# Performance work log

Measured on AMD Instinct MI355X. Metric: run time of the kernel, lower is better.

Reference implementation:

```python
import jax, jax.numpy as jnp
import numpy as np

B, N, D, H, O, K, N_USER, C = 1, 4096, 64, 4, 64, 2, 4000, 2


def setup_inputs() -> dict:
    key = jax.random.key(0)
    ks = jax.random.split(key, 7)
    h = jax.random.normal(ks[0], (B, N, D), jnp.float32)
    # dense 0/1 adjacency per heterogeneous kind, with self-loops so no row is empty
    adj = jax.random.randint(ks[1], (K, B, N, N), 0, 2).astype(jnp.float32)
    hadj = jnp.maximum(adj, jnp.eye(N, dtype=jnp.float32))
    s = 1.0 / np.sqrt(D).astype(np.float32)
    w = jax.random.normal(ks[2], (K, H, D, O), jnp.float32) * s
    a_src = jax.random.normal(ks[3], (K, H, O, 1), jnp.float32) * (1.0 / np.sqrt(O).astype(np.float32))
    a_dst = jax.random.normal(ks[4], (K, H, O, 1), jnp.float32) * (1.0 / np.sqrt(O).astype(np.float32))
    fc_w = jax.random.normal(ks[5], (C, O * K), jnp.float32) * (1.0 / np.sqrt(O * K).astype(np.float32))
    fc_b = jnp.zeros((C,), jnp.float32)
    return {"h": h, "hadj": hadj, "w": w, "a_src": a_src, "a_dst": a_dst, "fc_w": fc_w, "fc_b": fc_b}


def _gat(h, adj, w_k, a_src_k, a_dst_k):
    # h: (B,N,D); adj: (B,N,N); w_k: (H,D,O); a_*: (H,O,1)
    h_prime = jnp.einsum('bnf,hfo->bhno', h, w_k)          # (B,H,N,O)
    t = jnp.tanh(h_prime)
    attn_src = jnp.einsum('bhno,hoi->bhni', t, a_src_k)    # (B,H,N,1)
    attn_dst = jnp.einsum('bhno,hoi->bhni', t, a_dst_k)    # (B,H,N,1)
    attn = attn_src + jnp.swapaxes(attn_dst, -1, -2)       # (B,H,N,N) broadcast add
    attn = jnp.where(attn >= 0, attn, 0.2 * attn)          # LeakyReLU(0.2)
    attn = jnp.where(adj[:, None] > 0, attn, -jnp.inf)     # dense mask
    attn = jax.nn.softmax(attn, axis=-1)                   # dropout is a no-op in eval
    out = jnp.einsum('bhnm,bhmo->bhno', attn, h_prime)     # (B,H,N,O)
    return out.mean(axis=1)                                # mean over heads -> (B,N,O)


def reference(h, hadj, w, a_src, a_dst, fc_w, fc_b):
    embs = []
    for k in range(K):  # small fixed loop over heterogeneous node kinds
        x = _gat(h, hadj[k], w[k], a_src[k], a_dst[k])
        embs.append(x[:, :N_USER])
    type_aware = jnp.concatenate(embs, axis=-1)            # (B, N_USER, K*O)
    logits = type_aware @ fc_w.T + fc_b                    # (B, N_USER, C)
    return jax.nn.log_softmax(logits, axis=-1)
```

## Files before the change

### kernel.cpp

```cpp
#include <hip/hip_runtime.h>
#include <math.h>

constexpr int KK = 2;
constexpr int HH = 4;
constexpr int NN = 4096;
constexpr int DD = 64;
constexpr int OO = 64;
constexpr int NU = 4000;
constexpr int CC = 2;
constexpr float LOG2E = 1.44269504088896340736f;

typedef float vf4 __attribute__((ext_vector_type(4)));
typedef float vf2 __attribute__((ext_vector_type(2)));

__device__ __forceinline__ float fexp2(float x) {
#if __has_builtin(__builtin_amdgcn_exp2f)
  return __builtin_amdgcn_exp2f(x);
#else
  return exp2f(x);
#endif
}
__device__ __forceinline__ float frcp(float x) {
#if __has_builtin(__builtin_amdgcn_rcpf)
  return __builtin_amdgcn_rcpf(x);
#else
  return 1.0f / x;
#endif
}
__device__ __forceinline__ float ftanh(float x) {
  float e = fexp2(x * (2.0f * LOG2E));
  return 1.0f - 2.0f * frcp(e + 1.0f);
}

__global__ __launch_bounds__(256) void gat_phase1(
    const float* __restrict__ hsrc, const float* __restrict__ w,
    const float* __restrict__ a_src, const float* __restrict__ a_dst,
    const float* __restrict__ fc_w,
    float* __restrict__ srcAA, float* __restrict__ Bp,
    float* __restrict__ B5p, float* __restrict__ g0p,
    float* __restrict__ g1p) {
  const int kh = blockIdx.y;
  const int k = kh >> 2;
  const int i0 = blockIdx.x * 32;
  const int tid = threadIdx.x;

  __shared__ float w_s[DD][OO];
  __shared__ float hs_un[DD * 36];

  {
    const vf4* wp = (const vf4*)(w + (size_t)kh * DD * OO);
    vf4* ws4 = (vf4*)w_s;
    for (int t = tid; t < DD * OO / 4; t += 256) ws4[t] = wp[t];
  }
  for (int t = tid; t < 512; t += 256) {
    const int row = t >> 4;
    const int f4 = (t & 15) * 4;
    vf4 v = *(const vf4*)(hsrc + (size_t)(i0 + row) * DD + f4);
    hs_un[(f4 + 0) * 36 + row] = v.x;
    hs_un[(f4 + 1) * 36 + row] = v.y;
    hs_un[(f4 + 2) * 36 + row] = v.z;
    hs_un[(f4 + 3) * 36 + row] = v.w;
  }
  __syncthreads();

  const int og = tid & 15;
  const int rg = tid >> 4;
  const int o0 = og * 4;
  const int r0 = rg * 2;

  float hp[2][4];
#pragma unroll
  for (int j = 0; j < 2; ++j)
#pragma unroll
    for (int u = 0; u < 4; ++u) hp[j][u] = 0.0f;

#pragma unroll 8
  for (int f = 0; f < DD; ++f) {
    vf2 hv = *(const vf2*)&hs_un[f * 36 + r0];
    vf4 wv = *(const vf4*)&w_s[f][o0];
    hp[0][0] = fmaf(hv.x, wv.x, hp[0][0]);
    hp[0][1] = fmaf(hv.x, wv.y, hp[0][1]);
    hp[0][2] = fmaf(hv.x, wv.z, hp[0][2]);
    hp[0][3] = fmaf(hv.x, wv.w, hp[0][3]);
    hp[1][0] = fmaf(hv.y, wv.x, hp[1][0]);
    hp[1][1] = fmaf(hv.y, wv.y, hp[1][1]);
    hp[1][2] = fmaf(hv.y, wv.z, hp[1][2]);
    hp[1][3] = fmaf(hv.y, wv.w, hp[1][3]);
  }

  float as[4], ad[4], f0[4], f1[4];
#pragma unroll
  for (int u = 0; u < 4; ++u) {
    as[u] = a_src[kh * OO + o0 + u];
    ad[u] = a_dst[kh * OO + o0 + u];
    f0[u] = fc_w[0 * (KK * OO) + k * OO + o0 + u];
    f1[u] = fc_w[1 * (KK * OO) + k * OO + o0 + u];
  }

  float vals[2][4];
#pragma unroll
  for (int j = 0; j < 2; ++j) {
    float sp = 0.0f, dp = 0.0f, g0 = 0.0f, g1 = 0.0f;
#pragma unroll
    for (int u = 0; u < 4; ++u) {
      float v = hp[j][u];
      float t = ftanh(v);
      sp = fmaf(t, as[u], sp);
      dp = fmaf(t, ad[u], dp);
      g0 = fmaf(v, f0[u], g0);
      g1 = fmaf(v, f1[u], g1);
    }
    vals[j][0] = sp;
    vals[j][1] = dp;
    vals[j][2] = g0;
    vals[j][3] = g1;
  }
  __syncthreads();

#pragma unroll
  for (int j = 0; j < 2; ++j) {
#pragma unroll
    for (int v = 0; v < 4; ++v)
      hs_un[(v * 32 + r0 + j) * 17 + og] = vals[j][v];
  }
  __syncthreads();

  if (tid < 128) {
    const int val = tid & 3;
    const int j2 = tid >> 2;
    const float* pr = &hs_un[(val * 32 + j2) * 17];
    vf4 s0 = *(const vf4*)(pr + 0);
    vf4 s1 = *(const vf4*)(pr + 4);
    vf4 s2 = *(const vf4*)(pr + 8);
    vf4 s3 = *(const vf4*)(pr + 12);
    vf4 t4 = s0 + s1 + s2 + s3;
    float sum = t4.x + t4.y + t4.z + t4.w;
    const size_t idx = (size_t)kh * NN + i0 + j2;
    if (val == 0) {
      float sp = sum * LOG2E;
      vf2 v = {fexp2(sp), fexp2(0.2f * sp)};
      *(vf2*)(srcAA + idx * 2) = v;
    } else if (val == 1) {
      float dp = sum * LOG2E;
      Bp[idx] = fexp2(dp);
      B5p[idx] = fexp2(0.2f * dp);
    } else if (val == 2) {
      g0p[idx] = sum;
    } else {
      g1p[idx] = sum;
    }
  }
}

__global__ __launch_bounds__(256) void gat_phase2(
    const float* __restrict__ adj, const float* __restrict__ srcAA,
    const float* __restrict__ Bp, const float* __restrict__ B5p,
    const float* __restrict__ g0p, const float* __restrict__ g1p,
    float* __restrict__ S) {
  const int k = blockIdx.y;
  const int r0 = blockIdx.x * 4;
  const int tid = threadIdx.x;
  const int wave = tid >> 6;
  const int lane = tid & 63;

  float A[4][4], A5[4][4];
#pragma unroll
  for (int h = 0; h < 4; ++h) {
    const float* base = srcAA + ((size_t)(k * HH + h) * NN + r0) * 2;
#pragma unroll
    for (int r = 0; r < 4; ++r) {
      A[r][h] = base[r * 2 + 0];
      A5[r][h] = base[r * 2 + 1];
    }
  }

  float l[4][4], a0[4][4], a1[4][4];
#pragma unroll
  for (int r = 0; r < 4; ++r)
#pragma unroll
    for (int h = 0; h < 4; ++h) {
      l[r][h] = 0.0f;
      a0[r][h] = 0.0f;
      a1[r][h] = 0.0f;
    }

  const float* adjk = adj + (size_t)k * NN * NN;
  const int jw = wave * 1024 + lane * 4;

  vf4 avc[4], avn[4];
#pragma unroll
  for (int r = 0; r < 4; ++r)
    avc[r] = *(const vf4*)(adjk + (size_t)(r0 + r) * NN + jw);

#pragma unroll 1
  for (int t = 0; t < 4; ++t) {
    const int j = jw + t * 256;
    if (t < 3) {
#pragma unroll
      for (int r = 0; r < 4; ++r)
        avn[r] = *(const vf4*)(adjk + (size_t)(r0 + r) * NN + j + 256);
    }
    size_t pb = (size_t)(k * HH + 0) * NN + j;
    vf4 bC = *(const vf4*)(Bp + pb);
    vf4 b5C = *(const vf4*)(B5p + pb);
    vf4 g0C = *(const vf4*)(g0p + pb);
    vf4 g1C = *(const vf4*)(g1p + pb);
#pragma unroll
    for (int h = 0; h < 4; ++h) {
      vf4 b = bC, b5 = b5C, g0 = g0C, g1 = g1C;
      if (h < 3) {
        size_t pn = (size_t)(k * HH + h + 1) * NN + j;
        bC = *(const vf4*)(Bp + pn);
        b5C = *(const vf4*)(B5p + pn);
        g0C = *(const vf4*)(g0p + pn);
        g1C = *(const vf4*)(g1p + pn);
      }
      vf2 blo = {b.x, b.y}, bhi = {b.z, b.w};
      vf2 b5lo = {b5.x, b5.y}, b5hi = {b5.z, b5.w};
#pragma unroll
      for (int r = 0; r < 4; ++r) {
        vf2 elo = __builtin_elementwise_max(blo * A[r][h], b5lo * A5[r][h]);
        vf2 ehi = __builtin_elementwise_max(bhi * A[r][h], b5hi * A5[r][h]);
        float p0 = elo.x * avc[r].x;
        float p1 = elo.y * avc[r].y;
        float p2 = ehi.x * avc[r].z;
        float p3 = ehi.y * avc[r].w;
        l[r][h] += (p0 + p1) + (p2 + p3);
        a0[r][h] = fmaf(p0, g0.x, fmaf(p1, g0.y, fmaf(p2, g0.z, fmaf(p3, g0.w, a0[r][h]))));
        a1[r][h] = fmaf(p0, g1.x, fmaf(p1, g1.y, fmaf(p2, g1.z, fmaf(p3, g1.w, a1[r][h]))));
      }
    }
#pragma unroll
    for (int r = 0; r < 4; ++r) avc[r] = avn[r];
  }

  float red[4][4][3];
#pragma unroll
  for (int r = 0; r < 4; ++r)
#pragma unroll
    for (int h = 0; h < 4; ++h) {
      float x0 = l[r][h], x1 = a0[r][h], x2 = a1[r][h];
#pragma unroll
      for (int off = 32; off > 0; off >>= 1) {
        x0 += __shfl_xor(x0, off, 64);
        x1 += __shfl_xor(x1, off, 64);
        x2 += __shfl_xor(x2, off, 64);
      }
      red[r][h][0] = x0;
      red[r][h][1] = x1;
      red[r][h][2] = x2;
    }

  __shared__ float sred[4][48];
  if (lane == 0) {
#pragma unroll
    for (int r = 0; r < 4; ++r)
#pragma unroll
      for (int h = 0; h < 4; ++h) {
#pragma unroll
        for (int c = 0; c < 3; ++c)
          sred[wave][(r * 4 + h) * 3 + c] = red[r][h][c];
      }
  }
  __syncthreads();
  if (tid < 8) {
    const int r = tid >> 1, c = tid & 1;
    float acc = 0.0f;
#pragma unroll
    for (int h = 0; h < 4; ++h) {
      const int vb = (r * 4 + h) * 3;
      float ls = sred[0][vb] + sred[1][vb] + sred[2][vb] + sred[3][vb];
      float ac = sred[0][vb + 1 + c] + sred[1][vb + 1 + c] +
                 sred[2][vb + 1 + c] + sred[3][vb + 1 + c];
      acc += ac / ls;
    }
    S[((size_t)k * NU + r0 + r) * CC + c] = 0.25f * acc;
  }
}

__global__ __launch_bounds__(256) void gat_phase3(
    const float* __restrict__ S, const float* __restrict__ fc_b,
    float* __restrict__ out) {
  const int i = blockIdx.x * 256 + threadIdx.x;
  if (i >= NU) return;
  float l0 = S[(size_t)i * CC + 0] + S[((size_t)NU + i) * CC + 0] + fc_b[0];
  float l1 = S[(size_t)i * CC + 1] + S[((size_t)NU + i) * CC + 1] + fc_b[1];
  float m = fmaxf(l0, l1);
  float lse = m + logf(expf(l0 - m) + expf(l1 - m));
  out[i * CC + 0] = l0 - lse;
  out[i * CC + 1] = l1 - lse;
}

extern "C" void kernel_launch(void* const* d_in, const int* in_sizes, int n_in,
                              void* d_out, int out_size, void* d_ws, size_t ws_size,
                              hipStream_t stream) {
  const float* hsrc  = (const float*)d_in[0];
  const float* hadj  = (const float*)d_in[1];
  const float* w     = (const float*)d_in[2];
  const float* a_src = (const float*)d_in[3];
  const float* a_dst = (const float*)d_in[4];
  const float* fc_w  = (const float*)d_in[5];
  const float* fc_b  = (const float*)d_in[6];
  float* out = (float*)d_out;

  char* ws = (char*)d_ws;
  float* srcAA = (float*)(ws + 0);
  float* Bp    = (float*)(ws + 262144);
  float* B5p   = (float*)(ws + 393216);
  float* g0p   = (float*)(ws + 524288);
  float* g1p   = (float*)(ws + 655360);
  float* S     = (float*)(ws + 786432);

  dim3 g1(NN / 32, KK * HH);
  gat_phase1<<<g1, 256, 0, stream>>>(hsrc, w, a_src, a_dst, fc_w,
                                     srcAA, Bp, B5p, g0p, g1p);
  dim3 g2(NU / 4, KK);
  gat_phase2<<<g2, 256, 0, stream>>>(hadj, srcAA, Bp, B5p, g0p, g1p, S);
  gat_phase3<<<(NU + 255) / 256, 256, 0, stream>>>(S, fc_b, out);
}
```

Measured before the change: 235.6 us.

## Split phase2 into single-wave blocks per column chunk, reduce partials in phase3

Result: no change. 235.7 us (+0.1%).

```diff
diff --git a/kernel.cpp b/kernel.cpp
--- a/kernel.cpp
+++ b/kernel.cpp
@@ -8,6 +8,7 @@
 constexpr int OO = 64;
 constexpr int NU = 4000;
 constexpr int CC = 2;
+constexpr int JSPLIT = 4;
 constexpr float LOG2E = 1.44269504088896340736f;
 
 typedef float vf4 __attribute__((ext_vector_type(4)));
@@ -41,42 +42,43 @@
     float* __restrict__ g1p) {
   const int kh = blockIdx.y;
   const int k = kh >> 2;
-  const int i0 = blockIdx.x * 32;
+  const int i0 = blockIdx.x * 64;
   const int tid = threadIdx.x;
 
+  __shared__ float h_s[DD][68];
   __shared__ float w_s[DD][OO];
-  __shared__ float hs_un[DD * 36];
+  __shared__ float part[4][64][17];
 
   {
     const vf4* wp = (const vf4*)(w + (size_t)kh * DD * OO);
     vf4* ws4 = (vf4*)w_s;
     for (int t = tid; t < DD * OO / 4; t += 256) ws4[t] = wp[t];
   }
-  for (int t = tid; t < 512; t += 256) {
+  for (int t = tid; t < 1024; t += 256) {
     const int row = t >> 4;
     const int f4 = (t & 15) * 4;
     vf4 v = *(const vf4*)(hsrc + (size_t)(i0 + row) * DD + f4);
-    hs_un[(f4 + 0) * 36 + row] = v.x;
-    hs_un[(f4 + 1) * 36 + row] = v.y;
-    hs_un[(f4 + 2) * 36 + row] = v.z;
-    hs_un[(f4 + 3) * 36 + row] = v.w;
+    h_s[f4 + 0][row] = v.x;
+    h_s[f4 + 1][row] = v.y;
+    h_s[f4 + 2][row] = v.z;
+    h_s[f4 + 3][row] = v.w;
   }
   __syncthreads();
 
   const int og = tid & 15;
   const int rg = tid >> 4;
   const int o0 = og * 4;
-  const int r0 = rg * 2;
-
-  float hp[2][4];
-#pragma unroll
-  for (int j = 0; j < 2; ++j)
+  const int r0 = rg * 4;
+
+  float hp[4][4];
+#pragma unroll
+  for (int j = 0; j < 4; ++j)
 #pragma unroll
     for (int u = 0; u < 4; ++u) hp[j][u] = 0.0f;
 
 #pragma unroll 8
   for (int f = 0; f < DD; ++f) {
-    vf2 hv = *(const vf2*)&hs_un[f * 36 + r0];
+    vf4 hv = *(const vf4*)&h_s[f][r0];
     vf4 wv = *(const vf4*)&w_s[f][o0];
     hp[0][0] = fmaf(hv.x, wv.x, hp[0][0]);
     hp[0][1] = fmaf(hv.x, wv.y, hp[0][1]);
@@ -86,6 +88,14 @@
     hp[1][1] = fmaf(hv.y, wv.y, hp[1][1]);
     hp[1][2] = fmaf(hv.y, wv.z, hp[1][2]);
     hp[1][3] = fmaf(hv.y, wv.w, hp[1][3]);
+    hp[2][0] = fmaf(hv.z, wv.x, hp[2][0]);
+    hp[2][1] = fmaf(hv.z, wv.y, hp[2][1]);
+    hp[2][2] = fmaf(hv.z, wv.z, hp[2][2]);
+    hp[2][3] = fmaf(hv.z, wv.w, hp[2][3]);
+    hp[3][0] = fmaf(hv.w, wv.x, hp[3][0]);
+    hp[3][1] = fmaf(hv.w, wv.y, hp[3][1]);
+    hp[3][2] = fmaf(hv.w, wv.z, hp[3][2]);
+    hp[3][3] = fmaf(hv.w, wv.w, hp[3][3]);
   }
 
   float as[4], ad[4], f0[4], f1[4];
@@ -97,9 +107,8 @@
     f1[u] = fc_w[1 * (KK * OO) + k * OO + o0 + u];
   }
 
-  float vals[2][4];
-#pragma unroll
-  for (int j = 0; j < 2; ++j) {
+#pragma unroll
+  for (int j = 0; j < 4; ++j) {
     float sp = 0.0f, dp = 0.0f, g0 = 0.0f, g1 = 0.0f;
 #pragma unroll
     for (int u = 0; u < 4; ++u) {
@@ -110,25 +119,17 @@
       g0 = fmaf(v, f0[u], g0);
       g1 = fmaf(v, f1[u], g1);
     }
-    vals[j][0] = sp;
-    vals[j][1] = dp;
-    vals[j][2] = g0;
-    vals[j][3] = g1;
+    part[0][r0 + j][og] = sp;
+    part[1][r0 + j][og] = dp;
+    part[2][r0 + j][og] = g0;
+    part[3][r0 + j][og] = g1;
   }
   __syncthreads();
 
-#pragma unroll
-  for (int j = 0; j < 2; ++j) {
-#pragma unroll
-    for (int v = 0; v < 4; ++v)
-      hs_un[(v * 32 + r0 + j) * 17 + og] = vals[j][v];
-  }
-  __syncthreads();
-
-  if (tid < 128) {
+  {
     const int val = tid & 3;
     const int j2 = tid >> 2;
-    const float* pr = &hs_un[(val * 32 + j2) * 17];
+    const float* pr = &part[val][j2][0];
     vf4 s0 = *(const vf4*)(pr + 0);
     vf4 s1 = *(const vf4*)(pr + 4);
     vf4 s2 = *(const vf4*)(pr + 8);
@@ -152,16 +153,15 @@
   }
 }
 
-__global__ __launch_bounds__(256) void gat_phase2(
+__global__ __launch_bounds__(64) void gat_phase2(
     const float* __restrict__ adj, const float* __restrict__ srcAA,
     const float* __restrict__ Bp, const float* __restrict__ B5p,
     const float* __restrict__ g0p, const float* __restrict__ g1p,
-    float* __restrict__ S) {
-  const int k = blockIdx.y;
+    float* __restrict__ P) {
+  const int k = blockIdx.y >> 2;
+  const int chunk = blockIdx.y & 3;
   const int r0 = blockIdx.x * 4;
-  const int tid = threadIdx.x;
-  const int wave = tid >> 6;
-  const int lane = tid & 63;
+  const int lane = threadIdx.x;
 
   float A[4][4], A5[4][4];
 #pragma unroll
@@ -185,7 +185,7 @@
     }
 
   const float* adjk = adj + (size_t)k * NN * NN;
-  const int jw = wave * 1024 + lane * 4;
+  const int jw = chunk * 1024 + lane * 4;
 
   vf4 avc[4], avn[4];
 #pragma unroll
@@ -234,7 +234,6 @@
     for (int r = 0; r < 4; ++r) avc[r] = avn[r];
   }
 
-  float red[4][4][3];
 #pragma unroll
   for (int r = 0; r < 4; ++r)
 #pragma unroll
@@ -246,45 +245,48 @@
         x1 += __shfl_xor(x1, off, 64);
         x2 += __shfl_xor(x2, off, 64);
       }
-      red[r][h][0] = x0;
-      red[r][h][1] = x1;
-      red[r][h][2] = x2;
-    }
-
-  __shared__ float sred[4][48];
+      l[r][h] = x0;
+      a0[r][h] = x1;
+      a1[r][h] = x2;
+    }
+
   if (lane == 0) {
 #pragma unroll
     for (int r = 0; r < 4; ++r)
 #pragma unroll
       for (int h = 0; h < 4; ++h) {
-#pragma unroll
-        for (int c = 0; c < 3; ++c)
-          sred[wave][(r * 4 + h) * 3 + c] = red[r][h][c];
-      }
-  }
-  __syncthreads();
-  if (tid < 8) {
-    const int r = tid >> 1, c = tid & 1;
-    float acc = 0.0f;
-#pragma unroll
-    for (int h = 0; h < 4; ++h) {
-      const int vb = (r * 4 + h) * 3;
-      float ls = sred[0][vb] + sred[1][vb] + sred[2][vb] + sred[3][vb];
-      float ac = sred[0][vb + 1 + c] + sred[1][vb + 1 + c] +
-                 sred[2][vb + 1 + c] + sred[3][vb + 1 + c];
-      acc += ac / ls;
-    }
-    S[((size_t)k * NU + r0 + r) * CC + c] = 0.25f * acc;
+        size_t base =
+            (((size_t)(k * JSPLIT + chunk) * HH + h) * 3) * NU + (r0 + r);
+        P[base] = l[r][h];
+        P[base + NU] = a0[r][h];
+        P[base + 2 * (size_t)NU] = a1[r][h];
+      }
   }
 }
 
 __global__ __launch_bounds__(256) void gat_phase3(
-    const float* __restrict__ S, const float* __restrict__ fc_b,
+    const float* __restrict__ P, const float* __restrict__ fc_b,
     float* __restrict__ out) {
   const int i = blockIdx.x * 256 + threadIdx.x;
   if (i >= NU) return;
-  float l0 = S[(size_t)i * CC + 0] + S[((size_t)NU + i) * CC + 0] + fc_b[0];
-  float l1 = S[(size_t)i * CC + 1] + S[((size_t)NU + i) * CC + 1] + fc_b[1];
+  float l0 = fc_b[0], l1 = fc_b[1];
+#pragma unroll
+  for (int k = 0; k < KK; ++k) {
+#pragma unroll
+    for (int q = 0; q < HH; ++q) {
+      float ls = 0.0f, a0 = 0.0f, a1 = 0.0f;
+#pragma unroll
+      for (int ch = 0; ch < JSPLIT; ++ch) {
+        size_t b = (((size_t)(k * JSPLIT + ch) * HH + q) * 3) * NU + i;
+        ls += P[b];
+        a0 += P[b + NU];
+        a1 += P[b + 2 * (size_t)NU];
+      }
+      float inv = 1.0f / ls;
+      l0 = fmaf(0.25f * a0, inv, l0);
+      l1 = fmaf(0.25f * a1, inv, l1);
+    }
+  }
   float m = fmaxf(l0, l1);
   float lse = m + logf(expf(l0 - m) + expf(l1 - m));
   out[i * CC + 0] = l0 - lse;
@@ -309,12 +311,12 @@
   float* B5p   = (float*)(ws + 393216);
   float* g0p   = (float*)(ws + 524288);
   float* g1p   = (float*)(ws + 655360);
-  float* S     = (float*)(ws + 786432);
-
-  dim3 g1(NN / 32, KK * HH);
+  float* P     = (float*)(ws + 786432);
+
+  dim3 g1(NN / 64, KK * HH);
   gat_phase1<<<g1, 256, 0, stream>>>(hsrc, w, a_src, a_dst, fc_w,
                                      srcAA, Bp, B5p, g0p, g1p);
-  dim3 g2(NU / 4, KK);
-  gat_phase2<<<g2, 256, 0, stream>>>(hadj, srcAA, Bp, B5p, g0p, g1p, S);
-  gat_phase3<<<(NU + 255) / 256, 256, 0, stream>>>(S, fc_b, out);
-}
+  dim3 g2(NU / 4, KK * JSPLIT);
+  gat_phase2<<<g2, 64, 0, stream>>>(hadj, srcAA, Bp, B5p, g0p, g1p, P);
+  gat_phase3<<<(NU + 255) / 256, 256, 0, stream>>>(P, fc_b, out);
+}
```
